# Kernel optimization log

Hardware: AMD Instinct MI355X
Metric: run time of the kernel (lower is better)

Reference implementation:

```python
import jax, jax.numpy as jnp
import numpy as np

EPS = 1e-12  # torch F.normalize eps

def rmsnorm(x, g, dim):
    # F.normalize(x, dim=-1) * sqrt(dim) * g  (g is a learned scalar)
    n = jnp.maximum(jnp.linalg.norm(x, axis=-1, keepdims=True), EPS)
    return x / n * (dim ** 0.5) * g

def modulate(x, scale, shift):
    # x: (B,T,D); scale/shift: (B,D)
    return x * (1.0 + scale[:, None, :]) + shift[:, None, :]

def setup_inputs() -> dict:
    key = jax.random.key(0)
    ks = jax.random.split(key, 12)
    B, T, D, H = 8, 1024, 1024, 16
    Dm = 4 * D
    s = 0.02
    inp = {
        'x': jax.random.normal(ks[0], (B, T, D), jnp.float32),
        'c': jax.random.normal(ks[1], (B, D), jnp.float32),
        'g1': jnp.ones((1,), jnp.float32),
        'g2': jnp.ones((1,), jnp.float32),
        'gq': jnp.ones((1,), jnp.float32),
        'gk': jnp.ones((1,), jnp.float32),
        'Wqkv': jax.random.normal(ks[2], (3 * D, D), jnp.float32) * s,
        'bqkv': jnp.zeros((3 * D,), jnp.float32),
        'Wproj': jax.random.normal(ks[3], (D, D), jnp.float32) * s,
        'bproj': jnp.zeros((D,), jnp.float32),
        'Wfc1': jax.random.normal(ks[4], (Dm, D), jnp.float32) * s,
        'bfc1': jnp.zeros((Dm,), jnp.float32),
        'Wfc2': jax.random.normal(ks[5], (D, Dm), jnp.float32) * s,
        'bfc2': jnp.zeros((D,), jnp.float32),
        'Wada': jax.random.normal(ks[6], (6 * D, D), jnp.float32) * s,
        'bada': jnp.zeros((6 * D,), jnp.float32),
    }
    return inp

def reference(x, c, g1, g2, gq, gk, Wqkv, bqkv, Wproj, bproj,
              Wfc1, bfc1, Wfc2, bfc2, Wada, bada):
    B, T, D = x.shape
    H = 16
    hd = D // H

    # adaLN modulation: SiLU -> Linear -> chunk 6 along last dim
    ada = jax.nn.silu(c) @ Wada.T + bada  # (B, 6D)
    shift_msa, scale_msa, gate_msa, shift_mlp, scale_mlp, gate_mlp = jnp.split(ada, 6, axis=-1)

    # --- attention branch ---
    h = modulate(rmsnorm(x, g1, D), scale_msa, shift_msa)  # (B,T,D)
    qkv = h @ Wqkv.T + bqkv  # (B,T,3D)
    qkv = qkv.reshape(B, T, 3, H, hd).transpose(2, 0, 3, 1, 4)  # (3,B,H,T,hd)
    q, k, v = qkv[0], qkv[1], qkv[2]
    q = rmsnorm(q, gq, hd) * (hd ** -0.5)
    k = rmsnorm(k, gk, hd)
    attn = jax.nn.softmax(jnp.einsum('bhqd,bhkd->bhqk', q, k), axis=-1)
    o = jnp.einsum('bhqk,bhkd->bhqd', attn, v)  # (B,H,T,hd)
    o = o.transpose(0, 2, 1, 3).reshape(B, T, D)
    o = o @ Wproj.T + bproj
    x = x + gate_msa[:, None, :] * o

    # --- MLP branch ---
    h = modulate(rmsnorm(x, g2, D), scale_mlp, shift_mlp)
    h = jax.nn.gelu(h @ Wfc1.T + bfc1, approximate=True)
    h = h @ Wfc2.T + bfc2
    x = x + gate_mlp[:, None, :] * h
    return x
```

## Files before the change

### kernel.cpp

```cpp
#include <hip/hip_runtime.h>
#include <hip/hip_bf16.h>
#include <math.h>

typedef __bf16 bf16x8 __attribute__((ext_vector_type(8)));
typedef __bf16 bf16x4 __attribute__((ext_vector_type(4)));
typedef float  f32x4  __attribute__((ext_vector_type(4)));

#define DEV static __device__ __forceinline__

DEV unsigned short f2bf(float f) {
    unsigned u = __builtin_bit_cast(unsigned, f);
    u += 0x7fffu + ((u >> 16) & 1u);
    return (unsigned short)(u >> 16);
}
DEV float bf2f(unsigned short u) {
    unsigned x = ((unsigned)u) << 16;
    return __builtin_bit_cast(float, x);
}

__global__ void k_cvt(const float* __restrict__ in, unsigned short* __restrict__ out) {
    int i = (blockIdx.x * 256 + threadIdx.x) * 4;
    float4 v = *(const float4*)(in + i);
    ushort4 o;
    o.x = f2bf(v.x); o.y = f2bf(v.y); o.z = f2bf(v.z); o.w = f2bf(v.w);
    *(ushort4*)(out + i) = o;
}

__global__ void k_ada(const float* __restrict__ c, const float* __restrict__ Wada,
                      const float* __restrict__ bada, float* __restrict__ ada) {
    __shared__ float sc[1024];
    int b = blockIdx.x;
    int tid = threadIdx.x;
    for (int k = tid; k < 1024; k += 256) {
        float x = c[b * 1024 + k];
        sc[k] = x / (1.f + __expf(-x));
    }
    __syncthreads();
    int wid = tid >> 6, lane = tid & 63;
    int n = blockIdx.y * 4 + wid;
    const float* wr = Wada + (size_t)n * 1024;
    float acc = 0.f;
    #pragma unroll
    for (int k = 0; k < 1024; k += 64) acc += sc[k + lane] * wr[k + lane];
    #pragma unroll
    for (int o = 32; o; o >>= 1) acc += __shfl_xor(acc, o);
    if (lane == 0) ada[b * 6144 + n] = acc + bada[n];
}

__global__ void k_norm_mod(const float* __restrict__ x, const float* __restrict__ ada,
                           const float* __restrict__ g, unsigned short* __restrict__ h,
                           int shift_off, int scale_off) {
    int row = blockIdx.x;
    int b = row >> 10;
    int tid = threadIdx.x;
    float4 v = *(const float4*)(x + (size_t)row * 1024 + tid * 4);
    float ss = v.x * v.x + v.y * v.y + v.z * v.z + v.w * v.w;
    #pragma unroll
    for (int o = 32; o; o >>= 1) ss += __shfl_xor(ss, o);
    __shared__ float red[4];
    int wid = tid >> 6, lane = tid & 63;
    if (lane == 0) red[wid] = ss;
    __syncthreads();
    float nrm = sqrtf(red[0] + red[1] + red[2] + red[3]);
    float f = g[0] * 32.f / fmaxf(nrm, 1e-12f);
    float4 s4 = *(const float4*)(ada + b * 6144 + scale_off + tid * 4);
    float4 h4 = *(const float4*)(ada + b * 6144 + shift_off + tid * 4);
    ushort4 o;
    o.x = f2bf(v.x * f * (1.f + s4.x) + h4.x);
    o.y = f2bf(v.y * f * (1.f + s4.y) + h4.y);
    o.z = f2bf(v.z * f * (1.f + s4.z) + h4.z);
    o.w = f2bf(v.w * f * (1.f + s4.w) + h4.w);
    *(ushort4*)(h + (size_t)row * 1024 + tid * 4) = o;
}

template <int EPI>
__global__ __launch_bounds__(256, 4)
void k_gemm5(const unsigned short* __restrict__ A, const unsigned short* __restrict__ Bw,
             const float* __restrict__ bias, int N, int K, int gridM, int gridN, int Kc,
             unsigned short* __restrict__ outH) {
    __shared__ unsigned short lA[128 * 64];
    __shared__ unsigned short lB[128 * 64];
    int tid = threadIdx.x;
    int wid = tid >> 6, lane = tid & 63;
    int li = lane & 15, lg = lane >> 4;
    int bid = blockIdx.x;
    int mb = bid % gridM;
    int nb = (bid / gridM) % gridN;
    int sp = bid / (gridM * gridN);
    int m0 = mb * 128, n0 = nb * 128;
    int k0 = sp * Kc;
    int wr = (wid >> 1) * 64, wc = (wid & 1) * 64;

    int trow = tid >> 3;
    int gcol = ((tid & 7) ^ (trow & 7)) * 8;
    int sl0 = (lg ^ (li & 7)) * 8;
    int sl1 = ((4 + lg) ^ (li & 7)) * 8;

    f32x4 acc[4][4] = {};

    for (int kk = 0; kk < Kc; kk += 64) {
        #pragma unroll
        for (int l = 0; l < 4; ++l) {
            int row = l * 32 + trow;
            const unsigned short* ga = A  + (size_t)(m0 + row) * K + k0 + kk + gcol;
            const unsigned short* gb = Bw + (size_t)(n0 + row) * K + k0 + kk + gcol;
            unsigned short* la = lA + (l * 256 + wid * 64) * 8;
            unsigned short* lb = lB + (l * 256 + wid * 64) * 8;
            __builtin_amdgcn_global_load_lds((const __attribute__((address_space(1))) void*)ga,
                                             (__attribute__((address_space(3))) void*)la, 16, 0, 0);
            __builtin_amdgcn_global_load_lds((const __attribute__((address_space(1))) void*)gb,
                                             (__attribute__((address_space(3))) void*)lb, 16, 0, 0);
        }
        __syncthreads();
        bf16x8 af[4], bfr[4];
        #pragma unroll
        for (int i = 0; i < 4; ++i)
            af[i] = *(const bf16x8*)(lA + (wr + i * 16 + li) * 64 + sl0);
        #pragma unroll
        for (int j = 0; j < 4; ++j)
            bfr[j] = *(const bf16x8*)(lB + (wc + j * 16 + li) * 64 + sl0);
        #pragma unroll
        for (int i = 0; i < 4; ++i)
            #pragma unroll
            for (int j = 0; j < 4; ++j)
                acc[i][j] = __builtin_amdgcn_mfma_f32_16x16x32_bf16(af[i], bfr[j], acc[i][j], 0, 0, 0);
        #pragma unroll
        for (int i = 0; i < 4; ++i)
            af[i] = *(const bf16x8*)(lA + (wr + i * 16 + li) * 64 + sl1);
        #pragma unroll
        for (int j = 0; j < 4; ++j)
            bfr[j] = *(const bf16x8*)(lB + (wc + j * 16 + li) * 64 + sl1);
        #pragma unroll
        for (int i = 0; i < 4; ++i)
            #pragma unroll
            for (int j = 0; j < 4; ++j)
                acc[i][j] = __builtin_amdgcn_mfma_f32_16x16x32_bf16(af[i], bfr[j], acc[i][j], 0, 0, 0);
        __syncthreads();
    }

    int rb4 = lg * 4;
    size_t poff = (size_t)sp * ((size_t)8192 * N);
    #pragma unroll
    for (int i = 0; i < 4; ++i) {
        #pragma unroll
        for (int j = 0; j < 4; ++j) {
            #pragma unroll
            for (int r = 0; r < 4; ++r) {
                int row = m0 + wr + i * 16 + rb4 + r;
                int col = n0 + wc + j * 16 + li;
                if (EPI == 0) {
                    outH[(size_t)row * N + col] = f2bf(acc[i][j][r] + bias[col]);
                } else if (EPI == 2) {
                    float vv = acc[i][j][r] + bias[col];
                    float a2 = 0.7978845608f * (vv + 0.044715f * vv * vv * vv);
                    float e = __expf(-2.f * fabsf(a2));
                    float th = copysignf((1.f - e) / (1.f + e), a2);
                    outH[(size_t)row * N + col] = f2bf(0.5f * vv * (1.f + th));
                } else {
                    outH[poff + (size_t)row * N + col] = f2bf(acc[i][j][r]);
                }
            }
        }
    }
}

__global__ void k_fix_norm(const float* __restrict__ x, const unsigned short* __restrict__ P,
                           const float* __restrict__ bias, const float* __restrict__ ada,
                           const float* __restrict__ g2, float* __restrict__ out,
                           unsigned short* __restrict__ h2) {
    int row = blockIdx.x, b = row >> 10, tid = threadIdx.x;
    int c = tid * 4;
    size_t base = (size_t)row * 1024 + c;
    ushort4 p0 = *(const ushort4*)(P + base);
    ushort4 p1 = *(const ushort4*)(P + 8388608 + base);
    float4 xv = *(const float4*)(x + base);
    float4 bi = *(const float4*)(bias + c);
    float4 gt = *(const float4*)(ada + b * 6144 + 2048 + c);
    float4 v;
    v.x = xv.x + gt.x * (bf2f(p0.x) + bf2f(p1.x) + bi.x);
    v.y = xv.y + gt.y * (bf2f(p0.y) + bf2f(p1.y) + bi.y);
    v.z = xv.z + gt.z * (bf2f(p0.z) + bf2f(p1.z) + bi.z);
    v.w = xv.w + gt.w * (bf2f(p0.w) + bf2f(p1.w) + bi.w);
    *(float4*)(out + base) = v;
    float ss = v.x * v.x + v.y * v.y + v.z * v.z + v.w * v.w;
    #pragma unroll
    for (int o = 32; o; o >>= 1) ss += __shfl_xor(ss, o);
    __shared__ float red[4];
    int wid = tid >> 6, lane = tid & 63;
    if (lane == 0) red[wid] = ss;
    __syncthreads();
    float nrm = sqrtf(red[0] + red[1] + red[2] + red[3]);
    float f = g2[0] * 32.f / fmaxf(nrm, 1e-12f);
    float4 sc = *(const float4*)(ada + b * 6144 + 4096 + c);
    float4 sh = *(const float4*)(ada + b * 6144 + 3072 + c);
    ushort4 o;
    o.x = f2bf(v.x * f * (1.f + sc.x) + sh.x);
    o.y = f2bf(v.y * f * (1.f + sc.y) + sh.y);
    o.z = f2bf(v.z * f * (1.f + sc.z) + sh.z);
    o.w = f2bf(v.w * f * (1.f + sc.w) + sh.w);
    *(ushort4*)(h2 + base) = o;
}

__global__ void k_fixf(const unsigned short* __restrict__ P, const float* __restrict__ bias,
                       const float* __restrict__ ada, float* __restrict__ out) {
    int row = blockIdx.x, b = row >> 10, tid = threadIdx.x;
    int c = tid * 4;
    size_t base = (size_t)row * 1024 + c;
    ushort4 p0 = *(const ushort4*)(P + base);
    ushort4 p1 = *(const ushort4*)(P + 8388608 + base);
    float4 xv = *(const float4*)(out + base);
    float4 bi = *(const float4*)(bias + c);
    float4 gt = *(const float4*)(ada + b * 6144 + 5120 + c);
    float4 v;
    v.x = xv.x + gt.x * (bf2f(p0.x) + bf2f(p1.x) + bi.x);
    v.y = xv.y + gt.y * (bf2f(p0.y) + bf2f(p1.y) + bi.y);
    v.z = xv.z + gt.z * (bf2f(p0.z) + bf2f(p1.z) + bi.z);
    v.w = xv.w + gt.w * (bf2f(p0.w) + bf2f(p1.w) + bi.w);
    *(float4*)(out + base) = v;
}

__global__ __launch_bounds__(256)
void k_qkv_post(const unsigned short* __restrict__ qkv,
                const float* __restrict__ gq, const float* __restrict__ gk,
                unsigned short* __restrict__ Qb, unsigned short* __restrict__ Kb,
                unsigned short* __restrict__ Vtg) {
    __shared__ unsigned short vt[64 * 72];
    int bh = blockIdx.x;
    int b = bh >> 4, h = bh & 15;
    int t0 = blockIdx.y * 64;
    int tid = threadIdx.x;
    int row = tid >> 2, part = tid & 3;
    size_t rbase = ((size_t)(b * 1024 + t0 + row)) * 3072 + h * 64 + part * 16;
    size_t obase = (size_t)bh * 65536 + (size_t)(t0 + row) * 64 + part * 16;

    #pragma unroll
    for (int s = 0; s < 2; ++s) {
        uint4 u0 = *(const uint4*)(qkv + rbase + s * 1024);
        uint4 u1 = *(const uint4*)(qkv + rbase + s * 1024 + 8);
        float vals[16];
        const unsigned* pu = (const unsigned*)&u0;
        #pragma unroll
        for (int j = 0; j < 4; ++j) {
            vals[2*j]   = bf2f((unsigned short)(pu[j] & 0xffff));
            vals[2*j+1] = bf2f((unsigned short)(pu[j] >> 16));
        }
        pu = (const unsigned*)&u1;
        #pragma unroll
        for (int j = 0; j < 4; ++j) {
            vals[8+2*j]   = bf2f((unsigned short)(pu[j] & 0xffff));
            vals[8+2*j+1] = bf2f((unsigned short)(pu[j] >> 16));
        }
        float ss = 0.f;
        #pragma unroll
        for (int j = 0; j < 16; ++j) ss += vals[j] * vals[j];
        ss += __shfl_xor(ss, 1);
        ss += __shfl_xor(ss, 2);
        float nrm = fmaxf(sqrtf(ss), 1e-12f);
        float fsc = (s == 0 ? gq[0] : 8.f * gk[0]) / nrm;
        uint4 w0, w1;
        unsigned* pw = (unsigned*)&w0;
        #pragma unroll
        for (int j = 0; j < 4; ++j)
            pw[j] = (unsigned)f2bf(vals[2*j] * fsc) | ((unsigned)f2bf(vals[2*j+1] * fsc) << 16);
        pw = (unsigned*)&w1;
        #pragma unroll
        for (int j = 0; j < 4; ++j)
            pw[j] = (unsigned)f2bf(vals[8+2*j] * fsc) | ((unsigned)f2bf(vals[8+2*j+1] * fsc) << 16);
        unsigned short* dst = (s == 0 ? Qb : Kb);
        *(uint4*)(dst + obase)     = w0;
        *(uint4*)(dst + obase + 8) = w1;
    }
    {
        uint4 u0 = *(const uint4*)(qkv + rbase + 2048);
        uint4 u1 = *(const uint4*)(qkv + rbase + 2048 + 8);
        const unsigned* pu = (const unsigned*)&u0;
        #pragma unroll
        for (int j = 0; j < 4; ++j) {
            vt[(part * 16 + 2*j)     * 72 + row] = (unsigned short)(pu[j] & 0xffff);
            vt[(part * 16 + 2*j + 1) * 72 + row] = (unsigned short)(pu[j] >> 16);
        }
        pu = (const unsigned*)&u1;
        #pragma unroll
        for (int j = 0; j < 4; ++j) {
            vt[(part * 16 + 8 + 2*j)     * 72 + row] = (unsigned short)(pu[j] & 0xffff);
            vt[(part * 16 + 8 + 2*j + 1) * 72 + row] = (unsigned short)(pu[j] >> 16);
        }
    }
    __syncthreads();
    {
        int d = tid >> 2, seg = tid & 3;
        uint4 w0 = *(const uint4*)(vt + d * 72 + seg * 16);
        uint4 w1 = *(const uint4*)(vt + d * 72 + seg * 16 + 8);
        size_t vdst = (size_t)bh * 65536 + (size_t)d * 1024 + t0 + seg * 16;
        *(uint4*)(Vtg + vdst)     = w0;
        *(uint4*)(Vtg + vdst + 8) = w1;
    }
}

__global__ __launch_bounds__(256)
void k_attn_mfma(const unsigned short* __restrict__ Qb,
                 const unsigned short* __restrict__ Kb,
                 const unsigned short* __restrict__ Vtg,
                 unsigned short* __restrict__ outp) {
    __shared__ unsigned short Kt[128 * 64];
    __shared__ unsigned short Vl[64 * 136];
    int bh = blockIdx.x;
    int t0 = blockIdx.y * 64;
    int tid = threadIdx.x, wid = tid >> 6, lane = tid & 63;
    int li = lane & 15, lg = lane >> 4;
    const size_t bh64k = (size_t)bh * 65536;

    bf16x8 q0, q1;
    {
        const unsigned short* Qg = Qb + bh64k + (size_t)(t0 + wid * 16 + li) * 64 + lg * 8;
        q0 = *(const bf16x8*)Qg;
        q1 = *(const bf16x8*)(Qg + 32);
    }
    f32x4 oacc[4] = {};
    float den = 0.f;

    for (int kt = 0; kt < 8; ++kt) {
        __syncthreads();
        #pragma unroll
        for (int i = 0; i < 4; ++i) {
            int s = i * 256 + tid;
            int r = s >> 3, c16 = s & 7;
            const unsigned short* src = Kb + bh64k + (size_t)(kt * 128 + r) * 64 + ((c16 ^ (r & 7)) * 8);
            unsigned short* dst = Kt + i * 2048 + wid * 512;
            __builtin_amdgcn_global_load_lds((const __attribute__((address_space(1))) void*)src,
                                             (__attribute__((address_space(3))) void*)dst, 16, 0, 0);
        }
        #pragma unroll
        for (int i = 0; i < 4; ++i) {
            int s = i * 256 + tid;
            int d = s >> 4, k16 = s & 15;
            uint4 v = *(const uint4*)(Vtg + bh64k + (size_t)d * 1024 + kt * 128 + k16 * 8);
            *(uint4*)(Vl + d * 136 + k16 * 8) = v;
        }
        __syncthreads();

        f32x4 st[8];
        #pragma unroll
        for (int f = 0; f < 8; ++f) {
            int row = f * 16 + li;
            bf16x8 a0 = *(const bf16x8*)(Kt + row * 64 + ((lg       ^ (row & 7)) * 8));
            bf16x8 a1 = *(const bf16x8*)(Kt + row * 64 + (((4 + lg) ^ (row & 7)) * 8));
            f32x4 s = {};
            s = __builtin_amdgcn_mfma_f32_16x16x32_bf16(a0, q0, s, 0, 0, 0);
            s = __builtin_amdgcn_mfma_f32_16x16x32_bf16(a1, q1, s, 0, 0, 0);
            f32x4 e;
            e[0] = __expf(s[0]); e[1] = __expf(s[1]);
            e[2] = __expf(s[2]); e[3] = __expf(s[3]);
            den += e[0] + e[1] + e[2] + e[3];
            st[f] = e;
        }
        #pragma unroll
        for (int ks = 0; ks < 4; ++ks) {
            f32x4 e0 = st[2 * ks], e1 = st[2 * ks + 1];
            bf16x8 pa;
            pa[0] = (__bf16)e0[0]; pa[1] = (__bf16)e0[1]; pa[2] = (__bf16)e0[2]; pa[3] = (__bf16)e0[3];
            pa[4] = (__bf16)e1[0]; pa[5] = (__bf16)e1[1]; pa[6] = (__bf16)e1[2]; pa[7] = (__bf16)e1[3];
            #pragma unroll
            for (int df = 0; df < 4; ++df) {
                const unsigned short* vp = Vl + (df * 16 + li) * 136 + ks * 32 + lg * 4;
                bf16x4 v0 = *(const bf16x4*)vp;
                bf16x4 v1 = *(const bf16x4*)(vp + 16);
                bf16x8 vb = __builtin_shufflevector(v0, v1, 0, 1, 2, 3, 4, 5, 6, 7);
                oacc[df] = __builtin_amdgcn_mfma_f32_16x16x32_bf16(pa, vb, oacc[df], 0, 0, 0);
            }
        }
    }
    den += __shfl_xor(den, 16);
    den += __shfl_xor(den, 32);

    int b = bh >> 4, h = bh & 15;
    #pragma unroll
    for (int r2 = 0; r2 < 4; ++r2) {
        float dm = __shfl(den, lg * 4 + r2);
        float inv = 1.f / dm;
        int t = t0 + wid * 16 + lg * 4 + r2;
        #pragma unroll
        for (int df = 0; df < 4; ++df) {
            int col = h * 64 + df * 16 + li;
            outp[((size_t)(b * 1024 + t)) * 1024 + col] = f2bf(oacc[df][r2] * inv);
        }
    }
}

extern "C" void kernel_launch(void* const* d_in, const int* in_sizes, int n_in,
                              void* d_out, int out_size, void* d_ws, size_t ws_size,
                              hipStream_t stream) {
    const float* x     = (const float*)d_in[0];
    const float* c     = (const float*)d_in[1];
    const float* g1    = (const float*)d_in[2];
    const float* g2    = (const float*)d_in[3];
    const float* gq    = (const float*)d_in[4];
    const float* gk    = (const float*)d_in[5];
    const float* Wqkv  = (const float*)d_in[6];
    const float* bqkv  = (const float*)d_in[7];
    const float* Wproj = (const float*)d_in[8];
    const float* bproj = (const float*)d_in[9];
    const float* Wfc1  = (const float*)d_in[10];
    const float* bfc1  = (const float*)d_in[11];
    const float* Wfc2  = (const float*)d_in[12];
    const float* bfc2  = (const float*)d_in[13];
    const float* Wada  = (const float*)d_in[14];
    const float* bada  = (const float*)d_in[15];
    float* out = (float*)d_out;

    char* ws = (char*)d_ws;
    unsigned short* wqkv_bf = (unsigned short*)ws; ws += (size_t)3072 * 1024 * 2;
    unsigned short* wproj_bf= (unsigned short*)ws; ws += (size_t)1024 * 1024 * 2;
    unsigned short* wfc1_bf = (unsigned short*)ws; ws += (size_t)4096 * 1024 * 2;
    unsigned short* wfc2_bf = (unsigned short*)ws; ws += (size_t)4096 * 1024 * 2;
    float* ada = (float*)ws;                       ws += (size_t)8 * 6144 * 4;
    unsigned short* hbuf = (unsigned short*)ws;    ws += (size_t)8192 * 1024 * 2;
    unsigned short* qkvb16 = (unsigned short*)ws;  ws += (size_t)8192 * 3072 * 2;
    unsigned short* Qb  = (unsigned short*)ws;     ws += (size_t)8192 * 64 * 16 * 2;
    unsigned short* Kb  = (unsigned short*)ws;     ws += (size_t)8192 * 64 * 16 * 2;
    unsigned short* Vtg = (unsigned short*)ws;     ws += (size_t)8192 * 64 * 16 * 2;
    unsigned short* fc1out = qkvb16;
    unsigned short* Pp = Qb;
    unsigned short* Pf = Kb;

    k_cvt<<<3072 * 1024 / 1024, 256, 0, stream>>>(Wqkv,  wqkv_bf);
    k_cvt<<<1024 * 1024 / 1024, 256, 0, stream>>>(Wproj, wproj_bf);
    k_cvt<<<4096 * 1024 / 1024, 256, 0, stream>>>(Wfc1,  wfc1_bf);
    k_cvt<<<4096 * 1024 / 1024, 256, 0, stream>>>(Wfc2,  wfc2_bf);
    k_ada<<<dim3(8, 1536), 256, 0, stream>>>(c, Wada, bada, ada);
    k_norm_mod<<<8192, 256, 0, stream>>>(x, ada, g1, hbuf, 0, 1024);
    k_gemm5<0><<<1536, 256, 0, stream>>>(hbuf, wqkv_bf, bqkv, 3072, 1024, 64, 24, 1024, qkvb16);
    k_qkv_post<<<dim3(128, 16), 256, 0, stream>>>(qkvb16, gq, gk, Qb, Kb, Vtg);
    k_attn_mfma<<<dim3(128, 16), 256, 0, stream>>>(Qb, Kb, Vtg, hbuf);
    k_gemm5<4><<<1024, 256, 0, stream>>>(hbuf, wproj_bf, bproj, 1024, 1024, 64, 8, 512, Pp);
    k_fix_norm<<<8192, 256, 0, stream>>>(x, Pp, bproj, ada, g2, out, hbuf);
    k_gemm5<2><<<2048, 256, 0, stream>>>(hbuf, wfc1_bf, bfc1, 4096, 1024, 64, 32, 1024, fc1out);
    k_gemm5<4><<<1024, 256, 0, stream>>>(fc1out, wfc2_bf, bfc2, 1024, 4096, 64, 8, 2048, Pf);
    k_fixf<<<8192, 256, 0, stream>>>(Pf, bfc2, ada, out);
}
```

Measured before the change: 401.6 us.

## Fuse Q/K head RMSnorm into attention kernel and merge weight conversions

```diff
diff --git a/kernel.cpp b/kernel.cpp
--- a/kernel.cpp
+++ b/kernel.cpp
@@ -18,12 +18,20 @@
     return __builtin_bit_cast(float, x);
 }
 
-__global__ void k_cvt(const float* __restrict__ in, unsigned short* __restrict__ out) {
-    int i = (blockIdx.x * 256 + threadIdx.x) * 4;
-    float4 v = *(const float4*)(in + i);
+__global__ void k_cvtall(const float* __restrict__ a, const float* __restrict__ b,
+                         const float* __restrict__ c, const float* __restrict__ d,
+                         unsigned short* __restrict__ oa, unsigned short* __restrict__ ob,
+                         unsigned short* __restrict__ oc, unsigned short* __restrict__ od) {
+    size_t i = (size_t)blockIdx.x * 1024 + threadIdx.x * 4;
+    const float* src; unsigned short* dst; size_t off;
+    if (i < 3145728)      { src = a; dst = oa; off = i; }
+    else if (i < 4194304) { src = b; dst = ob; off = i - 3145728; }
+    else if (i < 8388608) { src = c; dst = oc; off = i - 4194304; }
+    else                  { src = d; dst = od; off = i - 8388608; }
+    float4 v = *(const float4*)(src + off);
     ushort4 o;
     o.x = f2bf(v.x); o.y = f2bf(v.y); o.z = f2bf(v.z); o.w = f2bf(v.w);
-    *(ushort4*)(out + i) = o;
+    *(ushort4*)(dst + off) = o;
 }
 
 __global__ void k_ada(const float* __restrict__ c, const float* __restrict__ Wada,
@@ -74,7 +82,7 @@
 }
 
 template <int EPI>
-__global__ __launch_bounds__(256, 4)
+__global__ __launch_bounds__(256, 5)
 void k_gemm5(const unsigned short* __restrict__ A, const unsigned short* __restrict__ Bw,
              const float* __restrict__ bias, int N, int K, int gridM, int gridN, int Kc,
              unsigned short* __restrict__ outH) {
@@ -220,91 +228,47 @@
 }
 
 __global__ __launch_bounds__(256)
-void k_qkv_post(const unsigned short* __restrict__ qkv,
-                const float* __restrict__ gq, const float* __restrict__ gk,
-                unsigned short* __restrict__ Qb, unsigned short* __restrict__ Kb,
-                unsigned short* __restrict__ Vtg) {
+void k_vt(const unsigned short* __restrict__ qkv, unsigned short* __restrict__ Vtg) {
     __shared__ unsigned short vt[64 * 72];
     int bh = blockIdx.x;
     int b = bh >> 4, h = bh & 15;
     int t0 = blockIdx.y * 64;
     int tid = threadIdx.x;
     int row = tid >> 2, part = tid & 3;
-    size_t rbase = ((size_t)(b * 1024 + t0 + row)) * 3072 + h * 64 + part * 16;
-    size_t obase = (size_t)bh * 65536 + (size_t)(t0 + row) * 64 + part * 16;
-
-    #pragma unroll
-    for (int s = 0; s < 2; ++s) {
-        uint4 u0 = *(const uint4*)(qkv + rbase + s * 1024);
-        uint4 u1 = *(const uint4*)(qkv + rbase + s * 1024 + 8);
-        float vals[16];
-        const unsigned* pu = (const unsigned*)&u0;
-        #pragma unroll
-        for (int j = 0; j < 4; ++j) {
-            vals[2*j]   = bf2f((unsigned short)(pu[j] & 0xffff));
-            vals[2*j+1] = bf2f((unsigned short)(pu[j] >> 16));
-        }
-        pu = (const unsigned*)&u1;
-        #pragma unroll
-        for (int j = 0; j < 4; ++j) {
-            vals[8+2*j]   = bf2f((unsigned short)(pu[j] & 0xffff));
-            vals[8+2*j+1] = bf2f((unsigned short)(pu[j] >> 16));
-        }
-        float ss = 0.f;
-        #pragma unroll
-        for (int j = 0; j < 16; ++j) ss += vals[j] * vals[j];
-        ss += __shfl_xor(ss, 1);
-        ss += __shfl_xor(ss, 2);
-        float nrm = fmaxf(sqrtf(ss), 1e-12f);
-        float fsc = (s == 0 ? gq[0] : 8.f * gk[0]) / nrm;
-        uint4 w0, w1;
-        unsigned* pw = (unsigned*)&w0;
-        #pragma unroll
-        for (int j = 0; j < 4; ++j)
-            pw[j] = (unsigned)f2bf(vals[2*j] * fsc) | ((unsigned)f2bf(vals[2*j+1] * fsc) << 16);
-        pw = (unsigned*)&w1;
-        #pragma unroll
-        for (int j = 0; j < 4; ++j)
-            pw[j] = (unsigned)f2bf(vals[8+2*j] * fsc) | ((unsigned)f2bf(vals[8+2*j+1] * fsc) << 16);
-        unsigned short* dst = (s == 0 ? Qb : Kb);
-        *(uint4*)(dst + obase)     = w0;
-        *(uint4*)(dst + obase + 8) = w1;
-    }
-    {
-        uint4 u0 = *(const uint4*)(qkv + rbase + 2048);
-        uint4 u1 = *(const uint4*)(qkv + rbase + 2048 + 8);
-        const unsigned* pu = (const unsigned*)&u0;
-        #pragma unroll
-        for (int j = 0; j < 4; ++j) {
-            vt[(part * 16 + 2*j)     * 72 + row] = (unsigned short)(pu[j] & 0xffff);
-            vt[(part * 16 + 2*j + 1) * 72 + row] = (unsigned short)(pu[j] >> 16);
-        }
-        pu = (const unsigned*)&u1;
-        #pragma unroll
-        for (int j = 0; j < 4; ++j) {
-            vt[(part * 16 + 8 + 2*j)     * 72 + row] = (unsigned short)(pu[j] & 0xffff);
-            vt[(part * 16 + 8 + 2*j + 1) * 72 + row] = (unsigned short)(pu[j] >> 16);
-        }
+    size_t rbase = ((size_t)(b * 1024 + t0 + row)) * 3072 + 2048 + h * 64 + part * 16;
+    uint4 u0 = *(const uint4*)(qkv + rbase);
+    uint4 u1 = *(const uint4*)(qkv + rbase + 8);
+    const unsigned* pu = (const unsigned*)&u0;
+    #pragma unroll
+    for (int j = 0; j < 4; ++j) {
+        vt[(part * 16 + 2*j)     * 72 + row] = (unsigned short)(pu[j] & 0xffff);
+        vt[(part * 16 + 2*j + 1) * 72 + row] = (unsigned short)(pu[j] >> 16);
+    }
+    pu = (const unsigned*)&u1;
+    #pragma unroll
+    for (int j = 0; j < 4; ++j) {
+        vt[(part * 16 + 8 + 2*j)     * 72 + row] = (unsigned short)(pu[j] & 0xffff);
+        vt[(part * 16 + 8 + 2*j + 1) * 72 + row] = (unsigned short)(pu[j] >> 16);
     }
     __syncthreads();
-    {
-        int d = tid >> 2, seg = tid & 3;
-        uint4 w0 = *(const uint4*)(vt + d * 72 + seg * 16);
-        uint4 w1 = *(const uint4*)(vt + d * 72 + seg * 16 + 8);
-        size_t vdst = (size_t)bh * 65536 + (size_t)d * 1024 + t0 + seg * 16;
-        *(uint4*)(Vtg + vdst)     = w0;
-        *(uint4*)(Vtg + vdst + 8) = w1;
-    }
+    int d = tid >> 2, seg = tid & 3;
+    uint4 w0 = *(const uint4*)(vt + d * 72 + seg * 16);
+    uint4 w1 = *(const uint4*)(vt + d * 72 + seg * 16 + 8);
+    size_t vdst = (size_t)bh * 65536 + (size_t)d * 1024 + t0 + seg * 16;
+    *(uint4*)(Vtg + vdst)     = w0;
+    *(uint4*)(Vtg + vdst + 8) = w1;
 }
 
 __global__ __launch_bounds__(256)
-void k_attn_mfma(const unsigned short* __restrict__ Qb,
-                 const unsigned short* __restrict__ Kb,
-                 const unsigned short* __restrict__ Vtg,
-                 unsigned short* __restrict__ outp) {
+void k_attn2(const unsigned short* __restrict__ qkv,
+             const unsigned short* __restrict__ Vtg,
+             const float* __restrict__ gq, const float* __restrict__ gk,
+             unsigned short* __restrict__ outp) {
     __shared__ unsigned short Kt[128 * 64];
     __shared__ unsigned short Vl[64 * 136];
+    __shared__ float normv[128];
     int bh = blockIdx.x;
+    int b = bh >> 4, h = bh & 15;
     int t0 = blockIdx.y * 64;
     int tid = threadIdx.x, wid = tid >> 6, lane = tid & 63;
     int li = lane & 15, lg = lane >> 4;
@@ -312,10 +276,26 @@
 
     bf16x8 q0, q1;
     {
-        const unsigned short* Qg = Qb + bh64k + (size_t)(t0 + wid * 16 + li) * 64 + lg * 8;
-        q0 = *(const bf16x8*)Qg;
-        q1 = *(const bf16x8*)(Qg + 32);
-    }
+        int qrow = b * 1024 + t0 + wid * 16 + li;
+        const unsigned short* Qg = qkv + (size_t)qrow * 3072 + h * 64 + lg * 8;
+        bf16x8 r0 = *(const bf16x8*)Qg;
+        bf16x8 r1 = *(const bf16x8*)(Qg + 32);
+        float ssq = 0.f;
+        #pragma unroll
+        for (int j = 0; j < 8; ++j) {
+            float a = (float)r0[j], bb = (float)r1[j];
+            ssq += a * a + bb * bb;
+        }
+        ssq += __shfl_xor(ssq, 16);
+        ssq += __shfl_xor(ssq, 32);
+        float qs = gq[0] / fmaxf(sqrtf(ssq), 1e-12f);
+        #pragma unroll
+        for (int j = 0; j < 8; ++j) {
+            q0[j] = (__bf16)((float)r0[j] * qs);
+            q1[j] = (__bf16)((float)r1[j] * qs);
+        }
+    }
+    float gk8 = 8.f * gk[0];
     f32x4 oacc[4] = {};
     float den = 0.f;
 
@@ -325,7 +305,8 @@
         for (int i = 0; i < 4; ++i) {
             int s = i * 256 + tid;
             int r = s >> 3, c16 = s & 7;
-            const unsigned short* src = Kb + bh64k + (size_t)(kt * 128 + r) * 64 + ((c16 ^ (r & 7)) * 8);
+            const unsigned short* src = qkv + (size_t)(b * 1024 + kt * 128 + r) * 3072
+                                        + 1024 + h * 64 + ((c16 ^ (r & 7)) * 8);
             unsigned short* dst = Kt + i * 2048 + wid * 512;
             __builtin_amdgcn_global_load_lds((const __attribute__((address_space(1))) void*)src,
                                              (__attribute__((address_space(3))) void*)dst, 16, 0, 0);
@@ -336,6 +317,19 @@
             int d = s >> 4, k16 = s & 15;
             uint4 v = *(const uint4*)(Vtg + bh64k + (size_t)d * 1024 + kt * 128 + k16 * 8);
             *(uint4*)(Vl + d * 136 + k16 * 8) = v;
+        }
+        __syncthreads();
+        {
+            int r = tid >> 1, hh = tid & 1;
+            float ss = 0.f;
+            #pragma unroll
+            for (int j = 0; j < 4; ++j) {
+                bf16x8 kv = *(const bf16x8*)(Kt + r * 64 + (((hh * 4 + j) ^ (r & 7)) * 8));
+                #pragma unroll
+                for (int u = 0; u < 8; ++u) { float a = (float)kv[u]; ss += a * a; }
+            }
+            ss += __shfl_xor(ss, 1);
+            if (!hh) normv[r] = gk8 / fmaxf(sqrtf(ss), 1e-12f);
         }
         __syncthreads();
 
@@ -348,9 +342,10 @@
             f32x4 s = {};
             s = __builtin_amdgcn_mfma_f32_16x16x32_bf16(a0, q0, s, 0, 0, 0);
             s = __builtin_amdgcn_mfma_f32_16x16x32_bf16(a1, q1, s, 0, 0, 0);
+            f32x4 nv = *(const f32x4*)(normv + f * 16 + lg * 4);
             f32x4 e;
-            e[0] = __expf(s[0]); e[1] = __expf(s[1]);
-            e[2] = __expf(s[2]); e[3] = __expf(s[3]);
+            e[0] = __expf(s[0] * nv[0]); e[1] = __expf(s[1] * nv[1]);
+            e[2] = __expf(s[2] * nv[2]); e[3] = __expf(s[3] * nv[3]);
             den += e[0] + e[1] + e[2] + e[3];
             st[f] = e;
         }
@@ -373,7 +368,6 @@
     den += __shfl_xor(den, 16);
     den += __shfl_xor(den, 32);
 
-    int b = bh >> 4, h = bh & 15;
     #pragma unroll
     for (int r2 = 0; r2 < 4; ++r2) {
         float dm = __shfl(den, lg * 4 + r2);
@@ -416,25 +410,20 @@
     float* ada = (float*)ws;                       ws += (size_t)8 * 6144 * 4;
     unsigned short* hbuf = (unsigned short*)ws;    ws += (size_t)8192 * 1024 * 2;
     unsigned short* qkvb16 = (unsigned short*)ws;  ws += (size_t)8192 * 3072 * 2;
-    unsigned short* Qb  = (unsigned short*)ws;     ws += (size_t)8192 * 64 * 16 * 2;
-    unsigned short* Kb  = (unsigned short*)ws;     ws += (size_t)8192 * 64 * 16 * 2;
     unsigned short* Vtg = (unsigned short*)ws;     ws += (size_t)8192 * 64 * 16 * 2;
+    unsigned short* Pbuf = (unsigned short*)ws;    ws += (size_t)2 * 8192 * 1024 * 2;
     unsigned short* fc1out = qkvb16;
-    unsigned short* Pp = Qb;
-    unsigned short* Pf = Kb;
-
-    k_cvt<<<3072 * 1024 / 1024, 256, 0, stream>>>(Wqkv,  wqkv_bf);
-    k_cvt<<<1024 * 1024 / 1024, 256, 0, stream>>>(Wproj, wproj_bf);
-    k_cvt<<<4096 * 1024 / 1024, 256, 0, stream>>>(Wfc1,  wfc1_bf);
-    k_cvt<<<4096 * 1024 / 1024, 256, 0, stream>>>(Wfc2,  wfc2_bf);
+
+    k_cvtall<<<12288, 256, 0, stream>>>(Wqkv, Wproj, Wfc1, Wfc2,
+                                        wqkv_bf, wproj_bf, wfc1_bf, wfc2_bf);
     k_ada<<<dim3(8, 1536), 256, 0, stream>>>(c, Wada, bada, ada);
     k_norm_mod<<<8192, 256, 0, stream>>>(x, ada, g1, hbuf, 0, 1024);
     k_gemm5<0><<<1536, 256, 0, stream>>>(hbuf, wqkv_bf, bqkv, 3072, 1024, 64, 24, 1024, qkvb16);
-    k_qkv_post<<<dim3(128, 16), 256, 0, stream>>>(qkvb16, gq, gk, Qb, Kb, Vtg);
-    k_attn_mfma<<<dim3(128, 16), 256, 0, stream>>>(Qb, Kb, Vtg, hbuf);
-    k_gemm5<4><<<1024, 256, 0, stream>>>(hbuf, wproj_bf, bproj, 1024, 1024, 64, 8, 512, Pp);
-    k_fix_norm<<<8192, 256, 0, stream>>>(x, Pp, bproj, ada, g2, out, hbuf);
+    k_vt<<<dim3(128, 16), 256, 0, stream>>>(qkvb16, Vtg);
+    k_attn2<<<dim3(128, 16), 256, 0, stream>>>(qkvb16, Vtg, gq, gk, hbuf);
+    k_gemm5<4><<<1024, 256, 0, stream>>>(hbuf, wproj_bf, bproj, 1024, 1024, 64, 8, 512, Pbuf);
+    k_fix_norm<<<8192, 256, 0, stream>>>(x, Pbuf, bproj, ada, g2, out, hbuf);
     k_gemm5<2><<<2048, 256, 0, stream>>>(hbuf, wfc1_bf, bfc1, 4096, 1024, 64, 32, 1024, fc1out);
-    k_gemm5<4><<<1024, 256, 0, stream>>>(fc1out, wfc2_bf, bfc2, 1024, 4096, 64, 8, 2048, Pf);
-    k_fixf<<<8192, 256, 0, stream>>>(Pf, bfc2, ada, out);
-}
+    k_gemm5<4><<<1024, 256, 0, stream>>>(fc1out, wfc2_bf, bfc2, 1024, 4096, 64, 8, 2048, Pbuf);
+    k_fixf<<<8192, 256, 0, stream>>>(Pbuf, bfc2, ada, out);
+}
```

New measurement: 731.7 us. 82.2% more time.
